# Kernel tuning notes

Hardware: AMD Instinct MI355X
Metric: run time of the kernel (lower is better)

## Reference

```python
import jax, jax.numpy as jnp
import numpy as np

NEG_SLOPE = 0.2   # PyG GATConv default negative_slope
BN_EPS = 1e-5
N_NODES = 50000
N_EDGES = 600000
N_GRAPHS = 64


def _gat_conv(x, W, att_src, att_dst, bias, src, dst, heads, out_ch, concat):
    """PyG GATConv (eval mode, self-loops already appended to src/dst).
    x: [N, in], W: [in, heads*out_ch], att_*: [heads, out_ch], bias: [heads*out_ch] or [out_ch].
    """
    n = x.shape[0]
    h = (x @ W).reshape(n, heads, out_ch)                  # [N, H, C]
    a_s = jnp.sum(h * att_src[None], axis=-1)              # [N, H]
    a_d = jnp.sum(h * att_dst[None], axis=-1)              # [N, H]
    logit = jax.nn.leaky_relu(a_s[src] + a_d[dst], NEG_SLOPE)  # [E, H]
    # segment softmax over destination node (every node has a self-loop -> no empty segment)
    m = jax.ops.segment_max(logit, dst, num_segments=n)
    p = jnp.exp(logit - m[dst])
    denom = jax.ops.segment_sum(p, dst, num_segments=n)
    alpha = p / (denom[dst] + 1e-16)                       # [E, H]
    out = jax.ops.segment_sum(h[src] * alpha[:, :, None], dst, num_segments=n)  # [N, H, C]
    out = out.reshape(n, heads * out_ch) if concat else out.mean(axis=1)
    return out + bias


def _bn(x, gamma, beta):
    mu = x.mean(axis=0)
    var = x.var(axis=0)
    return (x - mu) * jax.lax.rsqrt(var + BN_EPS) * gamma + beta


def setup_inputs() -> dict:
    key = jax.random.key(0)
    ks = jax.random.split(key, 20)
    hidden = 64
    d1_in, d1_out, h1 = 5, hidden // 2, 4          # 5 -> 32x4 = 128
    d2_in, d2_out, h2 = hidden * 2, hidden // 2, 4  # 128 -> 32x4 = 128
    d3_in, d3_out, h3 = hidden * 2, hidden, 1       # 128 -> 64

    def glorot(k, shape):
        fan = shape[0] + shape[-1]
        return jax.random.normal(k, shape, dtype=jnp.float32) * np.sqrt(2.0 / fan)

    inp = {
        "x": jax.random.normal(ks[0], (N_NODES, d1_in), dtype=jnp.float32),
        "edge_index": jax.random.randint(ks[1], (2, N_EDGES), 0, N_NODES),
        "batch": jnp.sort(jax.random.randint(ks[2], (N_NODES,), 0, N_GRAPHS)),
        # conv1
        "W1": glorot(ks[3], (d1_in, h1 * d1_out)),
        "a1_src": glorot(ks[4], (h1, d1_out)),
        "a1_dst": glorot(ks[5], (h1, d1_out)),
        "b1": jnp.zeros((h1 * d1_out,), dtype=jnp.float32),
        "g1": jnp.ones((h1 * d1_out,), dtype=jnp.float32),
        "be1": jnp.zeros((h1 * d1_out,), dtype=jnp.float32),
        # conv2
        "W2": glorot(ks[6], (d2_in, h2 * d2_out)),
        "a2_src": glorot(ks[7], (h2, d2_out)),
        "a2_dst": glorot(ks[8], (h2, d2_out)),
        "b2": jnp.zeros((h2 * d2_out,), dtype=jnp.float32),
        "g2": jnp.ones((h2 * d2_out,), dtype=jnp.float32),
        "be2": jnp.zeros((h2 * d2_out,), dtype=jnp.float32),
        # conv3 (single head, concat=False)
        "W3": glorot(ks[9], (d3_in, h3 * d3_out)),
        "a3_src": glorot(ks[10], (h3, d3_out)),
        "a3_dst": glorot(ks[11], (h3, d3_out)),
        "b3": jnp.zeros((d3_out,), dtype=jnp.float32),
    }
    return inp


def reference(x, edge_index, batch, W1, a1_src, a1_dst, b1, g1, be1,
              W2, a2_src, a2_dst, b2, g2, be2, W3, a3_src, a3_dst, b3):
    n = x.shape[0]
    loops = jnp.arange(n)
    src = jnp.concatenate([edge_index[0], loops])  # PyG add_self_loops=True
    dst = jnp.concatenate([edge_index[1], loops])

    h = jax.nn.elu(_bn(_gat_conv(x, W1, a1_src, a1_dst, b1, src, dst, 4, 32, True), g1, be1))
    h = jax.nn.elu(_bn(_gat_conv(h, W2, a2_src, a2_dst, b2, src, dst, 4, 32, True), g2, be2))
    h = jax.nn.elu(_gat_conv(h, W3, a3_src, a3_dst, b3, src, dst, 1, 64, False))

    counts = jax.ops.segment_sum(jnp.ones((n,), h.dtype), batch, num_segments=N_GRAPHS)
    mean_pool = jax.ops.segment_sum(h, batch, num_segments=N_GRAPHS) / jnp.maximum(counts, 1.0)[:, None]
    max_pool = jax.ops.segment_max(h, batch, num_segments=N_GRAPHS)
    max_pool = jnp.where(counts[:, None] > 0, max_pool, 0.0)
    return jnp.concatenate([mean_pool, max_pool], axis=1)  # [G, 128]
```

## Files before the change

kernel.cpp:

```cpp
#include <hip/hip_runtime.h>
#include <math.h>

#define NEG_SLOPE 0.2f
#define BN_EPS 1e-5f

typedef __attribute__((ext_vector_type(8))) short short8;
typedef __attribute__((ext_vector_type(4))) float f32x4;

__device__ __forceinline__ float lrelu_f(float x){ return x > 0.f ? x : NEG_SLOPE * x; }
__device__ __forceinline__ float elu_f(float x){ return x > 0.f ? x : __expf(x) - 1.f; }

__device__ __forceinline__ unsigned short f2bf(float f){
    unsigned u = __float_as_uint(f);
    return (unsigned short)((u + 0x7fffu + ((u >> 16) & 1u)) >> 16);
}
__device__ __forceinline__ float bf_lo(unsigned v){ return __uint_as_float(v << 16); }
__device__ __forceinline__ float bf_hi(unsigned v){ return __uint_as_float(v & 0xffff0000u); }
__device__ __forceinline__ float bf2f(unsigned short b){ return __uint_as_float((unsigned)b << 16); }

__device__ __forceinline__ unsigned enc_f(float x){
    unsigned b = __float_as_uint(x);
    return (b & 0x80000000u) ? ~b : (b | 0x80000000u);
}
__device__ __forceinline__ float dec_f(unsigned u){
    return __uint_as_float((u & 0x80000000u) ? (u & 0x7FFFFFFFu) : ~u);
}

__global__ void k_prep(const int* __restrict__ ei, int E0, int N, int Bc, int Bg,
                       const int* __restrict__ batch, int G,
                       int* __restrict__ counts, int* __restrict__ gp,
                       const float* __restrict__ W1, const float* __restrict__ a1s,
                       const float* __restrict__ a1d,
                       const float* __restrict__ W2, const float* __restrict__ W3,
                       unsigned short* __restrict__ wt2, unsigned short* __restrict__ wt3,
                       float* __restrict__ u_s, float* __restrict__ u_d){
    int b = blockIdx.x, tid = threadIdx.x;
    if (b < Bc){
        int i = b * 256 + tid, tot = E0 + N;
        if (i < tot){
            int dst = (i < E0) ? ei[E0 + i] : (i - E0);
            atomicAdd(&counts[dst], 1);
        }
    } else if (b < Bc + Bg){
        int i = (b - Bc) * 256 + tid;
        if (i < N){
            int bb = batch[i];
            if (i == 0){ for (int g = 0; g <= bb; ++g) gp[g] = 0; }
            else { int pb = batch[i - 1]; for (int g = pb + 1; g <= bb; ++g) gp[g] = i; }
            if (i == N - 1){ for (int g = bb + 1; g <= G; ++g) gp[g] = N; }
        }
    } else if (b < Bc + Bg + 96){
        int i = (b - Bc - Bg) * 256 + tid;
        if (i < 128 * 128){
            int k = i / 128, c = i % 128;
            wt2[c * 128 + k] = f2bf(W2[i]);
        } else if (i < 128 * 128 + 128 * 64){
            int j = i - 128 * 128;
            int k = j / 64, c = j % 64;
            wt3[c * 128 + k] = f2bf(W3[j]);
        }
    } else {
        if (tid < 40){
            int t2 = tid % 20;
            int k = t2 / 4, hh = t2 % 4;
            const float* att = (tid < 20) ? a1s : a1d;
            float s = 0.f;
            for (int j = 0; j < 32; ++j) s += W1[k * 128 + hh * 32 + j] * att[hh * 32 + j];
            if (tid < 20) u_s[k * 4 + hh] = s; else u_d[k * 4 + hh] = s;
        }
    }
}

__global__ void k_scan_part(const int* __restrict__ counts, int n, int* __restrict__ part){
    __shared__ int sh[256];
    int tid = threadIdx.x;
    int i = blockIdx.x * 256 + tid;
    int v = (i < n) ? counts[i] : 0;
    sh[tid] = v;
    __syncthreads();
    for (int o = 128; o > 0; o >>= 1){
        if (tid < o) sh[tid] += sh[tid + o];
        __syncthreads();
    }
    if (tid == 0) part[blockIdx.x] = sh[0];
}

__global__ void k_scan_write(const int* __restrict__ counts, const int* __restrict__ part,
                             int n, int* __restrict__ row_ptr){
    __shared__ int sh[256], rsh[256];
    __shared__ int offs;
    int tid = threadIdx.x, bid = blockIdx.x;
    int po = 0;
    for (int j = tid; j < bid; j += 256) po += part[j];
    rsh[tid] = po;
    __syncthreads();
    for (int o = 128; o > 0; o >>= 1){
        if (tid < o) rsh[tid] += rsh[tid + o];
        __syncthreads();
    }
    if (tid == 0) offs = rsh[0];
    __syncthreads();
    int i = bid * 256 + tid;
    int v = (i < n) ? counts[i] : 0;
    sh[tid] = v;
    __syncthreads();
    for (int o = 1; o < 256; o <<= 1){
        int t = (tid >= o) ? sh[tid - o] : 0;
        __syncthreads();
        sh[tid] += t;
        __syncthreads();
    }
    if (i < n) row_ptr[i] = offs + sh[tid] - v;
    if (bid == gridDim.x - 1 && tid == 255) row_ptr[n] = offs + sh[255];
}

__global__ void k_scatter(const int* __restrict__ ei, int E0, int N,
                          const int* __restrict__ row_ptr, int* __restrict__ cursor,
                          int* __restrict__ csr_src){
    int i = blockIdx.x * blockDim.x + threadIdx.x;
    int tot = E0 + N;
    if (i >= tot) return;
    int src, dst;
    if (i < E0){ src = ei[i]; dst = ei[E0 + i]; } else { src = dst = i - E0; }
    int pos = atomicAdd(&cursor[dst], 1);
    csr_src[row_ptr[dst] + pos] = src;
}

__launch_bounds__(256)
__global__ void k_l1(const float* __restrict__ X, const float* __restrict__ W1,
                     const float* __restrict__ u_s, const float* __restrict__ u_d,
                     const int* __restrict__ row_ptr, const int* __restrict__ csr_src,
                     const float* __restrict__ bias, float* __restrict__ out, int N){
    __shared__ float Wl[5 * 128];
    int tid = threadIdx.x;
    for (int i = tid; i < 5 * 128; i += 256) Wl[i] = W1[i];
    __syncthreads();
    int grp = tid >> 4, ln = tid & 15;
    int hh = ln >> 2, sl = ln & 3;
    long n = (long)blockIdx.x * 16 + grp;
    if (n >= N) return;
    float us[5], ud[5];
#pragma unroll
    for (int k = 0; k < 5; ++k){ us[k] = u_s[k * 4 + hh]; ud[k] = u_d[k * 4 + hh]; }
    float ad = 0.f;
#pragma unroll
    for (int k = 0; k < 5; ++k) ad += X[n * 5 + k] * ud[k];
    int beg = row_ptr[n], end = row_ptr[n + 1];
    float y0 = 0.f, y1 = 0.f, y2 = 0.f, y3 = 0.f, y4 = 0.f, dn = 0.f;
    for (int e = beg + sl; e < end; e += 4){
        long s = csr_src[e];
        float x0 = X[s * 5 + 0], x1 = X[s * 5 + 1], x2 = X[s * 5 + 2],
              x3 = X[s * 5 + 3], x4 = X[s * 5 + 4];
        float as = x0 * us[0] + x1 * us[1] + x2 * us[2] + x3 * us[3] + x4 * us[4];
        float p = __expf(lrelu_f(as + ad));
        dn += p;
        y0 += p * x0; y1 += p * x1; y2 += p * x2; y3 += p * x3; y4 += p * x4;
    }
#pragma unroll
    for (int m = 1; m < 4; m <<= 1){
        y0 += __shfl_xor(y0, m); y1 += __shfl_xor(y1, m); y2 += __shfl_xor(y2, m);
        y3 += __shfl_xor(y3, m); y4 += __shfl_xor(y4, m); dn += __shfl_xor(dn, m);
    }
    float inv = 1.f / dn;
    y0 *= inv; y1 *= inv; y2 *= inv; y3 *= inv; y4 *= inv;
    int c0 = ln * 8;
    const float4* Wl4 = (const float4*)Wl;
    float4 oa, ob;
    {
        float4 w0a = Wl4[0 * 32 + ln * 2], w0b = Wl4[0 * 32 + ln * 2 + 1];
        float4 w1a = Wl4[1 * 32 + ln * 2], w1b = Wl4[1 * 32 + ln * 2 + 1];
        float4 w2a = Wl4[2 * 32 + ln * 2], w2b = Wl4[2 * 32 + ln * 2 + 1];
        float4 w3a = Wl4[3 * 32 + ln * 2], w3b = Wl4[3 * 32 + ln * 2 + 1];
        float4 w4a = Wl4[4 * 32 + ln * 2], w4b = Wl4[4 * 32 + ln * 2 + 1];
        oa.x = y0*w0a.x + y1*w1a.x + y2*w2a.x + y3*w3a.x + y4*w4a.x + bias[c0 + 0];
        oa.y = y0*w0a.y + y1*w1a.y + y2*w2a.y + y3*w3a.y + y4*w4a.y + bias[c0 + 1];
        oa.z = y0*w0a.z + y1*w1a.z + y2*w2a.z + y3*w3a.z + y4*w4a.z + bias[c0 + 2];
        oa.w = y0*w0a.w + y1*w1a.w + y2*w2a.w + y3*w3a.w + y4*w4a.w + bias[c0 + 3];
        ob.x = y0*w0b.x + y1*w1b.x + y2*w2b.x + y3*w3b.x + y4*w4b.x + bias[c0 + 4];
        ob.y = y0*w0b.y + y1*w1b.y + y2*w2b.y + y3*w3b.y + y4*w4b.y + bias[c0 + 5];
        ob.z = y0*w0b.z + y1*w1b.z + y2*w2b.z + y3*w3b.z + y4*w4b.z + bias[c0 + 6];
        ob.w = y0*w0b.w + y1*w1b.w + y2*w2b.w + y3*w3b.w + y4*w4b.w + bias[c0 + 7];
    }
    *(float4*)&out[n * 128 + c0] = oa;
    *(float4*)&out[n * 128 + c0 + 4] = ob;
}

template<int OUT, int H, bool BN>
__launch_bounds__(256)
__global__ void k_gemm_mfma(const float* __restrict__ X, const unsigned short* __restrict__ Wt,
                            const float* __restrict__ atts, const float* __restrict__ attd,
                            const float* __restrict__ coefs, const float* __restrict__ coefb,
                            unsigned short* __restrict__ h, float* __restrict__ as_,
                            float* __restrict__ ad_, int N){
    constexpr int TM  = 64;
    constexpr int NCT = OUT / 16;
    constexpr int CPH = NCT / H;
    __shared__ unsigned short Xl[TM * 128];
    __shared__ unsigned short Wl[OUT * 128];
    int tid = threadIdx.x;
    long base = (long)blockIdx.x * TM;

    for (int i = tid; i < OUT * 16; i += 256){
        int r = i >> 4, g = i & 15;
        uint4 v = *(const uint4*)&Wt[r * 128 + g * 8];
        int gs = g ^ (r & 7);
        *(uint4*)&Wl[r * 128 + gs * 8] = v;
    }
    for (int i = tid; i < TM * 16; i += 256){
        int r = i >> 4, g = i & 15;
        long node = base + r;
        uint4 o;
        if (node < N){
            const float* xp = &X[node * 128 + g * 8];
            float f[8];
            *(float4*)&f[0] = *(const float4*)xp;
            *(float4*)&f[4] = *(const float4*)(xp + 4);
#pragma unroll
            for (int j = 0; j < 8; ++j){
                float v = f[j];
                if (BN) v = elu_f(fmaf(v, coefs[g * 8 + j], coefb[g * 8 + j]));
                f[j] = v;
            }
            o.x = (unsigned)f2bf(f[0]) | ((unsigned)f2bf(f[1]) << 16);
            o.y = (unsigned)f2bf(f[2]) | ((unsigned)f2bf(f[3]) << 16);
            o.z = (unsigned)f2bf(f[4]) | ((unsigned)f2bf(f[5]) << 16);
            o.w = (unsigned)f2bf(f[6]) | ((unsigned)f2bf(f[7]) << 16);
        } else {
            o.x = o.y = o.z = o.w = 0u;
        }
        int gs = g ^ (r & 7);
        *(uint4*)&Xl[r * 128 + gs * 8] = o;
    }
    __syncthreads();

    int wid = tid >> 6;
    int lane = tid & 63;
    int lr = lane & 15, lk = lane >> 4;

    short8 afrag[4];
    int arow = wid * 16 + lr;
#pragma unroll
    for (int ks = 0; ks < 4; ++ks){
        int g = ks * 4 + lk;
        int gs = g ^ (arow & 7);
        afrag[ks] = *(const short8*)&Xl[arow * 128 + gs * 8];
    }
    f32x4 acc[NCT];
#pragma unroll
    for (int ct = 0; ct < NCT; ++ct) acc[ct] = (f32x4){0.f, 0.f, 0.f, 0.f};
#pragma unroll
    for (int ct = 0; ct < NCT; ++ct){
        int brow = ct * 16 + lr;
#pragma unroll
        for (int ks = 0; ks < 4; ++ks){
            int g = ks * 4 + lk;
            int gs = g ^ (brow & 7);
            short8 bfrag = *(const short8*)&Wl[brow * 128 + gs * 8];
            acc[ct] = __builtin_amdgcn_mfma_f32_16x16x32_bf16(afrag[ks], bfrag, acc[ct], 0, 0, 0);
        }
    }
    float ps[H][4], pd[H][4];
#pragma unroll
    for (int hh = 0; hh < H; ++hh)
#pragma unroll
        for (int j = 0; j < 4; ++j){ ps[hh][j] = 0.f; pd[hh][j] = 0.f; }
#pragma unroll
    for (int ct = 0; ct < NCT; ++ct){
        int col = ct * 16 + lr;
        int hh = ct / CPH;
        float asv = atts[col], adv = attd[col];
#pragma unroll
        for (int j = 0; j < 4; ++j){
            float v = acc[ct][j];
            long node = base + wid * 16 + lk * 4 + j;
            if (node < N) h[node * OUT + col] = f2bf(v);
            ps[hh][j] += v * asv;
            pd[hh][j] += v * adv;
        }
    }
#pragma unroll
    for (int m = 1; m < 16; m <<= 1){
#pragma unroll
        for (int hh = 0; hh < H; ++hh)
#pragma unroll
            for (int j = 0; j < 4; ++j){
                ps[hh][j] += __shfl_xor(ps[hh][j], m);
                pd[hh][j] += __shfl_xor(pd[hh][j], m);
            }
    }
    if (lr == 0){
#pragma unroll
        for (int j = 0; j < 4; ++j){
            long node = base + wid * 16 + lk * 4 + j;
            if (node < N){
#pragma unroll
                for (int hh = 0; hh < H; ++hh){
                    as_[node * H + hh] = ps[hh][j];
                    ad_[node * H + hh] = pd[hh][j];
                }
            }
        }
    }
}

template<int C, int H, int ACT>
__global__ void k_agg(const unsigned short* __restrict__ h, const float* __restrict__ as_,
                      const float* __restrict__ ad_, const int* __restrict__ row_ptr,
                      const int* __restrict__ csr_src, const float* __restrict__ bias,
                      float* __restrict__ out, int N){
    constexpr int CPL = C / 64;
    constexpr int GROUP = C / H;
    int n = blockIdx.x;
    if (n >= N) return;
    int lane = threadIdx.x;
    int hh = (CPL * lane) / GROUP;
    float ad = ad_[n * H + hh];
    int beg = row_ptr[n], end = row_ptr[n + 1];
    float accx = 0.f, accy = 0.f, dn = 0.f;
    const unsigned* h32 = (const unsigned*)h;
    int e = beg;
    for (; e + 2 <= end; e += 2){
        int s0 = csr_src[e], s1 = csr_src[e + 1];
        float a0 = as_[s0 * H + hh], a1 = as_[s1 * H + hh];
        unsigned v0, v1; unsigned short w0, w1;
        if (CPL == 2){ v0 = h32[(long)s0 * 64 + lane]; v1 = h32[(long)s1 * 64 + lane]; }
        else { w0 = h[(long)s0 * 64 + lane]; w1 = h[(long)s1 * 64 + lane]; }
        float p0 = __expf(lrelu_f(a0 + ad));
        float p1 = __expf(lrelu_f(a1 + ad));
        dn += p0 + p1;
        if (CPL == 2){
            accx += p0 * bf_lo(v0) + p1 * bf_lo(v1);
            accy += p0 * bf_hi(v0) + p1 * bf_hi(v1);
        } else {
            accx += p0 * bf2f(w0) + p1 * bf2f(w1);
        }
    }
    if (e < end){
        int s0 = csr_src[e];
        float p0 = __expf(lrelu_f(as_[s0 * H + hh] + ad));
        dn += p0;
        if (CPL == 2){
            unsigned v0 = h32[(long)s0 * 64 + lane];
            accx += p0 * bf_lo(v0); accy += p0 * bf_hi(v0);
        } else {
            accx += p0 * bf2f(h[(long)s0 * 64 + lane]);
        }
    }
    float inv = 1.f / dn;
    if (CPL == 2){
        float vx = accx * inv + bias[2 * lane];
        float vy = accy * inv + bias[2 * lane + 1];
        if (ACT == 1){ vx = elu_f(vx); vy = elu_f(vy); }
        float2 o; o.x = vx; o.y = vy;
        *(float2*)&out[(long)n * C + 2 * lane] = o;
    } else {
        float v = accx * inv + bias[lane];
        if (ACT == 1) v = elu_f(v);
        out[(long)n * C + lane] = v;
    }
}

__launch_bounds__(256)
__global__ void k_bn_part(const float* __restrict__ x, int N,
                          float* __restrict__ ps, float* __restrict__ pq){
    __shared__ float4 lsum[256], lsq[256];
    int tid = threadIdx.x;
    int cq = tid & 31;
    int rg = tid >> 5;
    int rpb = (N + gridDim.x - 1) / gridDim.x;
    int lo = blockIdx.x * rpb;
    int hi = lo + rpb; if (hi > N) hi = N;
    float4 s = {0.f, 0.f, 0.f, 0.f}, q = {0.f, 0.f, 0.f, 0.f};
    int r = lo + rg;
    for (; r + 24 < hi; r += 32){
        float4 v0 = *(const float4*)&x[(long)r * 128 + cq * 4];
        float4 v1 = *(const float4*)&x[(long)(r + 8) * 128 + cq * 4];
        float4 v2 = *(const float4*)&x[(long)(r + 16) * 128 + cq * 4];
        float4 v3 = *(const float4*)&x[(long)(r + 24) * 128 + cq * 4];
        s.x += v0.x + v1.x + v2.x + v3.x;
        s.y += v0.y + v1.y + v2.y + v3.y;
        s.z += v0.z + v1.z + v2.z + v3.z;
        s.w += v0.w + v1.w + v2.w + v3.w;
        q.x += v0.x * v0.x + v1.x * v1.x + v2.x * v2.x + v3.x * v3.x;
        q.y += v0.y * v0.y + v1.y * v1.y + v2.y * v2.y + v3.y * v3.y;
        q.z += v0.z * v0.z + v1.z * v1.z + v2.z * v2.z + v3.z * v3.z;
        q.w += v0.w * v0.w + v1.w * v1.w + v2.w * v2.w + v3.w * v3.w;
    }
    for (; r < hi; r += 8){
        float4 v = *(const float4*)&x[(long)r * 128 + cq * 4];
        s.x += v.x; s.y += v.y; s.z += v.z; s.w += v.w;
        q.x += v.x * v.x; q.y += v.y * v.y; q.z += v.z * v.z; q.w += v.w * v.w;
    }
    lsum[tid] = s; lsq[tid] = q;
    __syncthreads();
    for (int o = 4; o > 0; o >>= 1){
        if (rg < o){
            float4 s2 = lsum[tid + o * 32], q2 = lsq[tid + o * 32];
            s.x += s2.x; s.y += s2.y; s.z += s2.z; s.w += s2.w;
            q.x += q2.x; q.y += q2.y; q.z += q2.z; q.w += q2.w;
            lsum[tid] = s; lsq[tid] = q;
        }
        __syncthreads();
    }
    if (rg == 0){
        *(float4*)&ps[(long)blockIdx.x * 128 + cq * 4] = s;
        *(float4*)&pq[(long)blockIdx.x * 128 + cq * 4] = q;
    }
}

__launch_bounds__(1024)
__global__ void k_bn_fin(const float* __restrict__ ps, const float* __restrict__ pq, int PB,
                         const float* __restrict__ g, const float* __restrict__ be,
                         float invN, float* __restrict__ cs, float* __restrict__ cb){
    __shared__ float sh_s[1024], sh_q[1024];
    int tid = threadIdx.x;
    int c = tid & 127, sl = tid >> 7;
    float s = 0.f, q = 0.f;
    for (int b = sl; b < PB; b += 8){
        s += ps[(long)b * 128 + c];
        q += pq[(long)b * 128 + c];
    }
    sh_s[tid] = s; sh_q[tid] = q;
    __syncthreads();
    for (int o = 4; o > 0; o >>= 1){
        if (sl < o){
            s += sh_s[tid + o * 128]; q += sh_q[tid + o * 128];
            sh_s[tid] = s; sh_q[tid] = q;
        }
        __syncthreads();
    }
    if (sl == 0){
        float mu = s * invN;
        float var = q * invN - mu * mu;
        float sc = g[c] * rsqrtf(var + BN_EPS);
        cs[c] = sc;
        cb[c] = be[c] - mu * sc;
    }
}

__global__ void k_pool_part(const float* __restrict__ x, const int* __restrict__ gp,
                            float* __restrict__ psum, unsigned* __restrict__ pmax){
    constexpr int S = 16;
    __shared__ float ssum[256], smax[256];
    int g = blockIdx.y;
    int split = blockIdx.x;
    int tid = threadIdx.x;
    int c = tid & 63, sub = tid >> 6;
    int beg = gp[g], end = gp[g + 1];
    int len = end - beg;
    int chunk = (len + S - 1) / S;
    int lo = beg + split * chunk;
    int hi = lo + chunk; if (hi > end) hi = end;
    if (lo >= hi) return;
    float s = 0.f, mx = -1e30f;
    for (int i = lo + sub; i < hi; i += 4){
        float v = x[(long)i * 64 + c];
        s += v; mx = fmaxf(mx, v);
    }
    ssum[tid] = s; smax[tid] = mx;
    __syncthreads();
    if (tid < 64){
        for (int k = 1; k < 4; ++k){ s += ssum[tid + 64 * k]; mx = fmaxf(mx, smax[tid + 64 * k]); }
        atomicAdd(&psum[g * 64 + c], s);
        atomicMax(&pmax[g * 64 + c], enc_f(mx));
    }
}

__global__ void k_pool_fin(const float* __restrict__ psum, const unsigned* __restrict__ pmax,
                           const int* __restrict__ gp, float* __restrict__ out){
    int g = blockIdx.x;
    int c = threadIdx.x;
    int cnt = gp[g + 1] - gp[g];
    float mean = (cnt > 0) ? psum[g * 64 + c] / (float)cnt : 0.f;
    float mx   = (cnt > 0) ? dec_f(pmax[g * 64 + c]) : 0.f;
    out[g * 128 + c]      = mean;
    out[g * 128 + 64 + c] = mx;
}

extern "C" void kernel_launch(void* const* d_in, const int* in_sizes, int n_in,
                              void* d_out, int out_size, void* d_ws, size_t ws_size,
                              hipStream_t stream){
    const float* x   = (const float*)d_in[0];
    const int*   ei  = (const int*)d_in[1];
    const int*   bat = (const int*)d_in[2];
    const float* W1  = (const float*)d_in[3];
    const float* a1s = (const float*)d_in[4];
    const float* a1d = (const float*)d_in[5];
    const float* b1  = (const float*)d_in[6];
    const float* g1  = (const float*)d_in[7];
    const float* be1 = (const float*)d_in[8];
    const float* W2  = (const float*)d_in[9];
    const float* a2s = (const float*)d_in[10];
    const float* a2d = (const float*)d_in[11];
    const float* b2  = (const float*)d_in[12];
    const float* g2  = (const float*)d_in[13];
    const float* be2 = (const float*)d_in[14];
    const float* W3  = (const float*)d_in[15];
    const float* a3s = (const float*)d_in[16];
    const float* a3d = (const float*)d_in[17];
    const float* b3  = (const float*)d_in[18];
    float* out = (float*)d_out;

    int N  = in_sizes[2];
    int E0 = in_sizes[1] / 2;
    int E  = E0 + N;
    const int G = 64;
    int P  = (N + 255) / 256;
    const int PB = 512;

    char* ws = (char*)d_ws;
    size_t off = 0;
    auto alloc = [&](size_t bytes) -> char* {
        char* p = ws + off;
        off += (bytes + 255) & ~(size_t)255;
        return p;
    };
    int*      counts  = (int*)alloc((size_t)N * 4);
    int*      cursor  = (int*)alloc((size_t)N * 4);
    float*    psum    = (float*)alloc((size_t)G * 64 * 4);
    unsigned* pmax    = (unsigned*)alloc((size_t)G * 64 * 4);
    size_t zero_bytes = off;
    int*   part    = (int*)alloc(256 * 4);
    int*   row_ptr = (int*)alloc((size_t)(N + 1) * 4);
    int*   csr     = (int*)alloc((size_t)E * 4);
    int*   gp      = (int*)alloc((size_t)(G + 1) * 4);
    float* as_buf  = (float*)alloc((size_t)N * 4 * 4);
    float* ad_buf  = (float*)alloc((size_t)N * 4 * 4);
    float* coefs   = (float*)alloc(128 * 4);
    float* coefb   = (float*)alloc(128 * 4);
    float* u_s     = (float*)alloc(20 * 4);
    float* u_d     = (float*)alloc(20 * 4);
    float* bn_ps   = (float*)alloc((size_t)PB * 128 * 4);
    float* bn_pq   = (float*)alloc((size_t)PB * 128 * 4);
    unsigned short* wt2 = (unsigned short*)alloc(128 * 128 * 2);
    unsigned short* wt3 = (unsigned short*)alloc(64 * 128 * 2);
    unsigned short* hbuf = (unsigned short*)alloc((size_t)N * 128 * 2);
    float* xcur    = (float*)alloc((size_t)N * 128 * 4);

    hipMemsetAsync(ws, 0, zero_bytes, stream);

    int Bc = (E + 255) / 256, Bg = (N + 255) / 256;
    k_prep<<<Bc + Bg + 96 + 1, 256, 0, stream>>>(ei, E0, N, Bc, Bg, bat, G, counts, gp,
                                                 W1, a1s, a1d, W2, W3, wt2, wt3, u_s, u_d);
    k_scan_part<<<P, 256, 0, stream>>>(counts, N, part);
    k_scan_write<<<P, 256, 0, stream>>>(counts, part, N, row_ptr);
    k_scatter<<<(E + 255) / 256, 256, 0, stream>>>(ei, E0, N, row_ptr, cursor, csr);

    k_l1<<<(N + 15) / 16, 256, 0, stream>>>(x, W1, u_s, u_d, row_ptr, csr, b1, xcur, N);
    k_bn_part<<<PB, 256, 0, stream>>>(xcur, N, bn_ps, bn_pq);
    k_bn_fin<<<1, 1024, 0, stream>>>(bn_ps, bn_pq, PB, g1, be1, 1.f / N, coefs, coefb);

    k_gemm_mfma<128, 4, true><<<(N + 63) / 64, 256, 0, stream>>>(
        xcur, wt2, a2s, a2d, coefs, coefb, hbuf, as_buf, ad_buf, N);
    k_agg<128, 4, 0><<<N, 64, 0, stream>>>(hbuf, as_buf, ad_buf, row_ptr, csr, b2, xcur, N);
    k_bn_part<<<PB, 256, 0, stream>>>(xcur, N, bn_ps, bn_pq);
    k_bn_fin<<<1, 1024, 0, stream>>>(bn_ps, bn_pq, PB, g2, be2, 1.f / N, coefs, coefb);

    k_gemm_mfma<64, 1, true><<<(N + 63) / 64, 256, 0, stream>>>(
        xcur, wt3, a3s, a3d, coefs, coefb, hbuf, as_buf, ad_buf, N);
    k_agg<64, 1, 1><<<N, 64, 0, stream>>>(hbuf, as_buf, ad_buf, row_ptr, csr, b3, xcur, N);

    {
        dim3 grid(16, G);
        k_pool_part<<<grid, 256, 0, stream>>>(xcur, gp, psum, pmax);
        k_pool_fin<<<G, 64, 0, stream>>>(psum, pmax, gp, out);
    }
}
```

Measured before the change: 242.5 us.

## Store intermediate layer activations in bf16 instead of fp32

Switches the inter-layer activation buffer (xcur) from fp32 to bf16. The layer-1 kernel and the aggregation kernels now write packed bf16. The GEMM, BatchNorm-partial and pooling kernels read bf16 and widen it to float. This halves the bytes moved for the activation write/read passes between stages, at the cost of rounding activations before BatchNorm statistics and pooling, which may affect accuracy.

```diff
diff --git a/kernel.cpp b/kernel.cpp
--- a/kernel.cpp
+++ b/kernel.cpp
@@ -130,7 +130,7 @@
 __global__ void k_l1(const float* __restrict__ X, const float* __restrict__ W1,
                      const float* __restrict__ u_s, const float* __restrict__ u_d,
                      const int* __restrict__ row_ptr, const int* __restrict__ csr_src,
-                     const float* __restrict__ bias, float* __restrict__ out, int N){
+                     const float* __restrict__ bias, unsigned short* __restrict__ out, int N){
     __shared__ float Wl[5 * 128];
     int tid = threadIdx.x;
     for (int i = tid; i < 5 * 128; i += 256) Wl[i] = W1[i];
@@ -181,13 +181,17 @@
         ob.z = y0*w0b.z + y1*w1b.z + y2*w2b.z + y3*w3b.z + y4*w4b.z + bias[c0 + 6];
         ob.w = y0*w0b.w + y1*w1b.w + y2*w2b.w + y3*w3b.w + y4*w4b.w + bias[c0 + 7];
     }
-    *(float4*)&out[n * 128 + c0] = oa;
-    *(float4*)&out[n * 128 + c0 + 4] = ob;
+    uint4 o;
+    o.x = (unsigned)f2bf(oa.x) | ((unsigned)f2bf(oa.y) << 16);
+    o.y = (unsigned)f2bf(oa.z) | ((unsigned)f2bf(oa.w) << 16);
+    o.z = (unsigned)f2bf(ob.x) | ((unsigned)f2bf(ob.y) << 16);
+    o.w = (unsigned)f2bf(ob.z) | ((unsigned)f2bf(ob.w) << 16);
+    *(uint4*)&out[n * 128 + c0] = o;
 }
 
 template<int OUT, int H, bool BN>
 __launch_bounds__(256)
-__global__ void k_gemm_mfma(const float* __restrict__ X, const unsigned short* __restrict__ Wt,
+__global__ void k_gemm_mfma(const unsigned short* __restrict__ X, const unsigned short* __restrict__ Wt,
                             const float* __restrict__ atts, const float* __restrict__ attd,
                             const float* __restrict__ coefs, const float* __restrict__ coefb,
                             unsigned short* __restrict__ h, float* __restrict__ as_,
@@ -211,10 +215,12 @@
         long node = base + r;
         uint4 o;
         if (node < N){
-            const float* xp = &X[node * 128 + g * 8];
+            uint4 raw = *(const uint4*)&X[node * 128 + g * 8];
             float f[8];
-            *(float4*)&f[0] = *(const float4*)xp;
-            *(float4*)&f[4] = *(const float4*)(xp + 4);
+            f[0] = bf_lo(raw.x); f[1] = bf_hi(raw.x);
+            f[2] = bf_lo(raw.y); f[3] = bf_hi(raw.y);
+            f[4] = bf_lo(raw.z); f[5] = bf_hi(raw.z);
+            f[6] = bf_lo(raw.w); f[7] = bf_hi(raw.w);
 #pragma unroll
             for (int j = 0; j < 8; ++j){
                 float v = f[j];
@@ -307,7 +313,7 @@
 __global__ void k_agg(const unsigned short* __restrict__ h, const float* __restrict__ as_,
                       const float* __restrict__ ad_, const int* __restrict__ row_ptr,
                       const int* __restrict__ csr_src, const float* __restrict__ bias,
-                      float* __restrict__ out, int N){
+                      unsigned short* __restrict__ out, int N){
     constexpr int CPL = C / 64;
     constexpr int GROUP = C / H;
     int n = blockIdx.x;
@@ -351,60 +357,71 @@
         float vx = accx * inv + bias[2 * lane];
         float vy = accy * inv + bias[2 * lane + 1];
         if (ACT == 1){ vx = elu_f(vx); vy = elu_f(vy); }
-        float2 o; o.x = vx; o.y = vy;
-        *(float2*)&out[(long)n * C + 2 * lane] = o;
+        ((unsigned*)out)[(long)n * 64 + lane] =
+            (unsigned)f2bf(vx) | ((unsigned)f2bf(vy) << 16);
     } else {
         float v = accx * inv + bias[lane];
         if (ACT == 1) v = elu_f(v);
-        out[(long)n * C + lane] = v;
+        out[(long)n * 64 + lane] = f2bf(v);
     }
 }
 
 __launch_bounds__(256)
-__global__ void k_bn_part(const float* __restrict__ x, int N,
+__global__ void k_bn_part(const unsigned short* __restrict__ x, int N,
                           float* __restrict__ ps, float* __restrict__ pq){
-    __shared__ float4 lsum[256], lsq[256];
+    __shared__ float ls[256 * 8], lq[256 * 8];
     int tid = threadIdx.x;
-    int cq = tid & 31;
-    int rg = tid >> 5;
+    int cg = tid & 15;
+    int rg = tid >> 4;
     int rpb = (N + gridDim.x - 1) / gridDim.x;
     int lo = blockIdx.x * rpb;
     int hi = lo + rpb; if (hi > N) hi = N;
-    float4 s = {0.f, 0.f, 0.f, 0.f}, q = {0.f, 0.f, 0.f, 0.f};
+    float s[8], q[8];
+#pragma unroll
+    for (int j = 0; j < 8; ++j){ s[j] = 0.f; q[j] = 0.f; }
     int r = lo + rg;
-    for (; r + 24 < hi; r += 32){
-        float4 v0 = *(const float4*)&x[(long)r * 128 + cq * 4];
-        float4 v1 = *(const float4*)&x[(long)(r + 8) * 128 + cq * 4];
-        float4 v2 = *(const float4*)&x[(long)(r + 16) * 128 + cq * 4];
-        float4 v3 = *(const float4*)&x[(long)(r + 24) * 128 + cq * 4];
-        s.x += v0.x + v1.x + v2.x + v3.x;
-        s.y += v0.y + v1.y + v2.y + v3.y;
-        s.z += v0.z + v1.z + v2.z + v3.z;
-        s.w += v0.w + v1.w + v2.w + v3.w;
-        q.x += v0.x * v0.x + v1.x * v1.x + v2.x * v2.x + v3.x * v3.x;
-        q.y += v0.y * v0.y + v1.y * v1.y + v2.y * v2.y + v3.y * v3.y;
-        q.z += v0.z * v0.z + v1.z * v1.z + v2.z * v2.z + v3.z * v3.z;
-        q.w += v0.w * v0.w + v1.w * v1.w + v2.w * v2.w + v3.w * v3.w;
-    }
-    for (; r < hi; r += 8){
-        float4 v = *(const float4*)&x[(long)r * 128 + cq * 4];
-        s.x += v.x; s.y += v.y; s.z += v.z; s.w += v.w;
-        q.x += v.x * v.x; q.y += v.y * v.y; q.z += v.z * v.z; q.w += v.w * v.w;
-    }
-    lsum[tid] = s; lsq[tid] = q;
-    __syncthreads();
-    for (int o = 4; o > 0; o >>= 1){
+    for (; r + 16 < hi; r += 32){
+        uint4 va = *(const uint4*)&x[(long)r * 128 + cg * 8];
+        uint4 vb = *(const uint4*)&x[(long)(r + 16) * 128 + cg * 8];
+        float fa[8], fb[8];
+        fa[0]=bf_lo(va.x); fa[1]=bf_hi(va.x); fa[2]=bf_lo(va.y); fa[3]=bf_hi(va.y);
+        fa[4]=bf_lo(va.z); fa[5]=bf_hi(va.z); fa[6]=bf_lo(va.w); fa[7]=bf_hi(va.w);
+        fb[0]=bf_lo(vb.x); fb[1]=bf_hi(vb.x); fb[2]=bf_lo(vb.y); fb[3]=bf_hi(vb.y);
+        fb[4]=bf_lo(vb.z); fb[5]=bf_hi(vb.z); fb[6]=bf_lo(vb.w); fb[7]=bf_hi(vb.w);
+#pragma unroll
+        for (int j = 0; j < 8; ++j){
+            s[j] += fa[j] + fb[j];
+            q[j] += fa[j] * fa[j] + fb[j] * fb[j];
+        }
+    }
+    for (; r < hi; r += 16){
+        uint4 va = *(const uint4*)&x[(long)r * 128 + cg * 8];
+        float fa[8];
+        fa[0]=bf_lo(va.x); fa[1]=bf_hi(va.x); fa[2]=bf_lo(va.y); fa[3]=bf_hi(va.y);
+        fa[4]=bf_lo(va.z); fa[5]=bf_hi(va.z); fa[6]=bf_lo(va.w); fa[7]=bf_hi(va.w);
+#pragma unroll
+        for (int j = 0; j < 8; ++j){ s[j] += fa[j]; q[j] += fa[j] * fa[j]; }
+    }
+#pragma unroll
+    for (int j = 0; j < 8; ++j){ ls[tid * 8 + j] = s[j]; lq[tid * 8 + j] = q[j]; }
+    __syncthreads();
+    for (int o = 8; o > 0; o >>= 1){
         if (rg < o){
-            float4 s2 = lsum[tid + o * 32], q2 = lsq[tid + o * 32];
-            s.x += s2.x; s.y += s2.y; s.z += s2.z; s.w += s2.w;
-            q.x += q2.x; q.y += q2.y; q.z += q2.z; q.w += q2.w;
-            lsum[tid] = s; lsq[tid] = q;
+#pragma unroll
+            for (int j = 0; j < 8; ++j){
+                s[j] += ls[(tid + o * 16) * 8 + j];
+                q[j] += lq[(tid + o * 16) * 8 + j];
+                ls[tid * 8 + j] = s[j]; lq[tid * 8 + j] = q[j];
+            }
         }
         __syncthreads();
     }
     if (rg == 0){
-        *(float4*)&ps[(long)blockIdx.x * 128 + cq * 4] = s;
-        *(float4*)&pq[(long)blockIdx.x * 128 + cq * 4] = q;
+#pragma unroll
+        for (int j = 0; j < 8; ++j){
+            ps[(long)blockIdx.x * 128 + cg * 8 + j] = s[j];
+            pq[(long)blockIdx.x * 128 + cg * 8 + j] = q[j];
+        }
     }
 }
 
@@ -438,31 +455,44 @@
     }
 }
 
-__global__ void k_pool_part(const float* __restrict__ x, const int* __restrict__ gp,
+__global__ void k_pool_part(const unsigned short* __restrict__ x, const int* __restrict__ gp,
                             float* __restrict__ psum, unsigned* __restrict__ pmax){
     constexpr int S = 16;
-    __shared__ float ssum[256], smax[256];
+    __shared__ float2 ssum[256], smax[256];
     int g = blockIdx.y;
     int split = blockIdx.x;
     int tid = threadIdx.x;
-    int c = tid & 63, sub = tid >> 6;
+    int c2 = tid & 31, sub = tid >> 5;
     int beg = gp[g], end = gp[g + 1];
     int len = end - beg;
     int chunk = (len + S - 1) / S;
     int lo = beg + split * chunk;
     int hi = lo + chunk; if (hi > end) hi = end;
     if (lo >= hi) return;
-    float s = 0.f, mx = -1e30f;
-    for (int i = lo + sub; i < hi; i += 4){
-        float v = x[(long)i * 64 + c];
-        s += v; mx = fmaxf(mx, v);
-    }
-    ssum[tid] = s; smax[tid] = mx;
-    __syncthreads();
-    if (tid < 64){
-        for (int k = 1; k < 4; ++k){ s += ssum[tid + 64 * k]; mx = fmaxf(mx, smax[tid + 64 * k]); }
-        atomicAdd(&psum[g * 64 + c], s);
-        atomicMax(&pmax[g * 64 + c], enc_f(mx));
+    float sx = 0.f, sy = 0.f, mx = -1e30f, my = -1e30f;
+    const unsigned* xr = (const unsigned*)x;
+    for (int i = lo + sub; i < hi; i += 8){
+        unsigned v = xr[(long)i * 32 + c2];
+        float a = bf_lo(v), b = bf_hi(v);
+        sx += a; sy += b;
+        mx = fmaxf(mx, a); my = fmaxf(my, b);
+    }
+    ssum[tid] = make_float2(sx, sy); smax[tid] = make_float2(mx, my);
+    __syncthreads();
+    for (int o = 4; o > 0; o >>= 1){
+        if (sub < o){
+            float2 s2 = ssum[tid + o * 32], m2 = smax[tid + o * 32];
+            sx += s2.x; sy += s2.y;
+            mx = fmaxf(mx, m2.x); my = fmaxf(my, m2.y);
+            ssum[tid] = make_float2(sx, sy); smax[tid] = make_float2(mx, my);
+        }
+        __syncthreads();
+    }
+    if (sub == 0){
+        atomicAdd(&psum[g * 64 + c2 * 2], sx);
+        atomicAdd(&psum[g * 64 + c2 * 2 + 1], sy);
+        atomicMax(&pmax[g * 64 + c2 * 2], enc_f(mx));
+        atomicMax(&pmax[g * 64 + c2 * 2 + 1], enc_f(my));
     }
 }
 
@@ -535,7 +565,7 @@
     unsigned short* wt2 = (unsigned short*)alloc(128 * 128 * 2);
     unsigned short* wt3 = (unsigned short*)alloc(64 * 128 * 2);
     unsigned short* hbuf = (unsigned short*)alloc((size_t)N * 128 * 2);
-    float* xcur    = (float*)alloc((size_t)N * 128 * 4);
+    unsigned short* xcur = (unsigned short*)alloc((size_t)N * 128 * 2);
 
     hipMemsetAsync(ws, 0, zero_bytes, stream);
 
```

Result: faster. 233.1 us (-3.8%).
